# Optimization experiments

Hardware: AMD Instinct MI355X
Metric: run time of the kernel (lower is better)

Reference implementation:

```python
import jax, jax.numpy as jnp
import numpy as np

B, INDIM, ENC, BOT, DEC = 2048, 20000, 512, 128, 512
EPS = 1e-5


def _bn(x, g, b):
    # BatchNorm1d in training mode: biased batch stats
    m = jnp.mean(x, axis=0)
    v = jnp.mean(jnp.square(x - m), axis=0)
    return (x - m) * jax.lax.rsqrt(v + EPS) * g + b


def setup_inputs() -> dict:
    key = jax.random.key(0)
    ks = jax.random.split(key, 8)
    s = 0.02  # small init scale keeps exp() outputs finite
    return {
        "x": jax.random.uniform(ks[0], (B, INDIM), dtype=jnp.float32),
        "bn0_g": jnp.ones((INDIM,), jnp.float32),
        "bn0_b": jnp.zeros((INDIM,), jnp.float32),
        "enc_W": jax.random.normal(ks[1], (ENC, INDIM), jnp.float32) * s,
        "enc_b": jnp.zeros((ENC,), jnp.float32),
        "bn1_g": jnp.ones((ENC,), jnp.float32),
        "bn1_b": jnp.zeros((ENC,), jnp.float32),
        "bot_W": jax.random.normal(ks[2], (BOT, ENC), jnp.float32) * s,
        "bot_b": jnp.zeros((BOT,), jnp.float32),
        "bn2_g": jnp.ones((BOT,), jnp.float32),
        "bn2_b": jnp.zeros((BOT,), jnp.float32),
        "dec_W": jax.random.normal(ks[3], (DEC, BOT), jnp.float32) * s,
        "dec_b": jnp.zeros((DEC,), jnp.float32),
        "o1_W": jax.random.normal(ks[4], (INDIM, DEC), jnp.float32) * s,
        "o1_b": jnp.zeros((INDIM,), jnp.float32),
        "o2_W": jax.random.normal(ks[5], (INDIM, DEC), jnp.float32) * s,
        "o2_b": jnp.zeros((INDIM,), jnp.float32),
        "o3_W": jax.random.normal(ks[6], (INDIM, DEC), jnp.float32) * s,
        "o3_b": jnp.zeros((INDIM,), jnp.float32),
    }


def reference(x, bn0_g, bn0_b, enc_W, enc_b, bn1_g, bn1_b, bot_W, bot_b,
              bn2_g, bn2_b, dec_W, dec_b, o1_W, o1_b, o2_W, o2_b, o3_W, o3_b):
    # row-sum / median normalization; diag-inverse @ x == x / s[:, None]
    row_sum = jnp.sum(x, axis=1)                     # [B]
    s = row_sum / jnp.median(row_sum)                # [B]
    h = jnp.log1p(x / s[:, None])                    # log(inv(diag(s)) @ x + 1)
    h = _bn(h, bn0_g, bn0_b)
    h = jax.nn.relu(h @ enc_W.T + enc_b)
    h = _bn(h, bn1_g, bn1_b)
    h = jax.nn.relu(h @ bot_W.T + bot_b)
    h = _bn(h, bn2_g, bn2_b)
    h = jax.nn.relu(h @ dec_W.T + dec_b)
    M = jnp.exp(h @ o1_W.T + o1_b)
    M_loss = s[:, None] * M                          # diag(s) @ M
    pai = jax.nn.sigmoid(h @ o2_W.T + o2_b)
    theta = jnp.exp(h @ o3_W.T + o3_b)
    return pai, M, theta, M_loss
```

## Files before the change

kernel.cpp:

```cpp
#include <hip/hip_runtime.h>
#include <hip/hip_bf16.h>
#include <math.h>

#define B_    2048
#define IND   20000
#define ENCN  512
#define BOTN  128
#define DECN  512
#define KP1   20480
#define NP    20224
#define SPLITK 16
#define KSTEP1 20
#define BNEPS 1e-5f

typedef __hip_bfloat16 bf16;
typedef __bf16 bf16x8 __attribute__((ext_vector_type(8)));
typedef float f32x4 __attribute__((ext_vector_type(4)));
typedef unsigned short u16;

__device__ __forceinline__ u16 f2bfu(float f) {
  __hip_bfloat16 h = __float2bfloat16(f);
  return *reinterpret_cast<u16*>(&h);
}

__device__ __forceinline__ void gload_lds16(const bf16* g, bf16* l) {
  __builtin_amdgcn_global_load_lds(
      (const __attribute__((address_space(1))) void*)g,
      (__attribute__((address_space(3))) void*)l, 16, 0, 0);
}

__global__ void rowsum_k(const float* __restrict__ x, float* __restrict__ row_sum) {
  const int row = blockIdx.x;
  const f32x4* xr = (const f32x4*)(x + (size_t)row * IND);
  float s = 0.f;
  for (int i = threadIdx.x; i < IND / 4; i += 256) {
    f32x4 v = xr[i];
    s += (v[0] + v[1]) + (v[2] + v[3]);
  }
#pragma unroll
  for (int o = 32; o > 0; o >>= 1) s += __shfl_down(s, o, 64);
  __shared__ float ws4[4];
  if ((threadIdx.x & 63) == 0) ws4[threadIdx.x >> 6] = s;
  __syncthreads();
  if (threadIdx.x == 0) row_sum[row] = (ws4[0] + ws4[1]) + (ws4[2] + ws4[3]);
}

__global__ void median_scale_k(const float* __restrict__ row_sum,
                               float* __restrict__ sArr, float* __restrict__ invs) {
  __shared__ float v[B_];
  const int tid = threadIdx.x;
  v[tid] = row_sum[tid];
  v[tid + 1024] = row_sum[tid + 1024];
  __syncthreads();
  for (int k = 2; k <= B_; k <<= 1) {
    for (int j = k >> 1; j > 0; j >>= 1) {
      for (int i = tid; i < B_; i += 1024) {
        int ixj = i ^ j;
        if (ixj > i) {
          bool up = ((i & k) == 0);
          float a = v[i], b = v[ixj];
          if ((a > b) == up) { v[i] = b; v[ixj] = a; }
        }
      }
      __syncthreads();
    }
  }
  float med = 0.5f * (v[B_ / 2 - 1] + v[B_ / 2]);
  for (int i = tid; i < B_; i += 1024) {
    float rs = row_sum[i];
    sArr[i] = rs / med;
    invs[i] = med / rs;
  }
}

__global__ void pass2_k(const float* __restrict__ x, const float* __restrict__ invs,
                        bf16* __restrict__ L, float* __restrict__ part_s,
                        float* __restrict__ part_q) {
  const int c0 = (blockIdx.x * 256 + threadIdx.x) * 4;
  const int rblk = blockIdx.y;
  const int r0 = rblk * 32;
  const bool valid = (c0 < IND);
  f32x4 sum = {0.f, 0.f, 0.f, 0.f}, sq = {0.f, 0.f, 0.f, 0.f};
  for (int r = r0; r < r0 + 32; ++r) {
    f32x4 lv = {0.f, 0.f, 0.f, 0.f};
    if (valid) {
      f32x4 v = *(const f32x4*)(x + (size_t)r * IND + c0);
      float iv = invs[r];
      lv[0] = log1pf(v[0] * iv); lv[1] = log1pf(v[1] * iv);
      lv[2] = log1pf(v[2] * iv); lv[3] = log1pf(v[3] * iv);
      sum += lv; sq += lv * lv;
    }
    ushort4 o;
    o.x = f2bfu(lv[0]); o.y = f2bfu(lv[1]); o.z = f2bfu(lv[2]); o.w = f2bfu(lv[3]);
    *(ushort4*)((u16*)L + (size_t)r * KP1 + c0) = o;
  }
  if (valid) {
    *(f32x4*)(part_s + (size_t)rblk * KP1 + c0) = sum;
    *(f32x4*)(part_q + (size_t)rblk * KP1 + c0) = sq;
  }
}

__global__ void finalize_bn_k(const float* __restrict__ part_s, const float* __restrict__ part_q,
                              const float* __restrict__ g, const float* __restrict__ b,
                              float* __restrict__ scale, float* __restrict__ shift) {
  int c = blockIdx.x * 256 + threadIdx.x;
  if (c >= IND) return;
  float s = 0.f, q = 0.f;
  for (int z = 0; z < 64; ++z) {
    s += part_s[(size_t)z * KP1 + c];
    q += part_q[(size_t)z * KP1 + c];
  }
  const float invN = 1.f / (float)B_;
  float mean = s * invN;
  float var = q * invN - mean * mean;
  float sc = g[c] * rsqrtf(var + BNEPS);
  scale[c] = sc;
  shift[c] = b[c] - mean * sc;
}

__global__ void prepw_k(const float* __restrict__ encW, const float* __restrict__ enc_b,
                        const float* __restrict__ scale0, const float* __restrict__ shift0,
                        bf16* __restrict__ Wp, float* __restrict__ bias1) {
  const int e = blockIdx.x;
  float local = 0.f;
  for (int j0 = threadIdx.x * 4; j0 < KP1; j0 += 1024) {
    ushort4 o;
    if (j0 < IND) {
      f32x4 w = *(const f32x4*)(encW + (size_t)e * IND + j0);
      f32x4 sc = *(const f32x4*)(scale0 + j0);
      f32x4 sh = *(const f32x4*)(shift0 + j0);
      local += sh[0] * w[0] + sh[1] * w[1] + sh[2] * w[2] + sh[3] * w[3];
      o.x = f2bfu(w[0] * sc[0]); o.y = f2bfu(w[1] * sc[1]);
      o.z = f2bfu(w[2] * sc[2]); o.w = f2bfu(w[3] * sc[3]);
    } else {
      o.x = 0; o.y = 0; o.z = 0; o.w = 0;
    }
    *(ushort4*)((u16*)Wp + (size_t)e * KP1 + j0) = o;
  }
#pragma unroll
  for (int o = 32; o > 0; o >>= 1) local += __shfl_down(local, o, 64);
  __shared__ float red[4];
  if ((threadIdx.x & 63) == 0) red[threadIdx.x >> 6] = local;
  __syncthreads();
  if (threadIdx.x == 0) bias1[e] = enc_b[e] + ((red[0] + red[1]) + (red[2] + red[3]));
}

template <int MODE>
__global__ __launch_bounds__(512, 2)
void gemm256(const bf16* __restrict__ A, const bf16* __restrict__ Bm,
             int Kpad, int ksteps,
             float* __restrict__ out0, float* __restrict__ out1,
             const float* __restrict__ bias, const float* __restrict__ sArr,
             int ldo, int Nlimit) {
  extern __shared__ __align__(16) bf16 smem[];
  bf16* AsB = smem;
  bf16* BsB = smem + 32768;
  const int tid = threadIdx.x;
  const int lane = tid & 63;
  const int wave = tid >> 6;
  const int wr = wave >> 2;
  const int wc = wave & 3;

  const int nwg = gridDim.x;
  const int q8 = nwg >> 3;
  const int bid = blockIdx.x;
  const int swz = (bid & 7) * q8 + (bid >> 3);
  const int xm = swz & 7;
  const int rest = swz >> 3;
  int yn, z;
  if (MODE == 0) { yn = rest & 1; z = rest >> 1; } else { yn = rest; z = 0; }
  const int m0 = xm * 256;
  const int n0 = yn * 256;
  const int kbeg = z * ksteps * 64;

  const int srow = tid >> 3;
  const int schunk = (tid & 7) ^ (srow & 7);
  const bf16* gA = A + (size_t)(m0 + srow) * Kpad + kbeg + schunk * 8;
  const bf16* gB = Bm + (size_t)(n0 + srow) * Kpad + kbeg + schunk * 8;
  const int ldst = tid * 8;

  f32x4 acc[8][4] = {};
  const int lrow = lane & 15;
  const int kq = lane >> 4;

  auto STAGE = [&](int ks, int buf) {
    const bf16* ga = gA + (size_t)ks * 64;
    const bf16* gb = gB + (size_t)ks * 64;
    bf16* la = AsB + buf * 16384 + ldst;
    bf16* lb = BsB + buf * 16384 + ldst;
#pragma unroll
    for (int i = 0; i < 4; ++i) {
      gload_lds16(ga + (size_t)(i * 64) * Kpad, la + i * 4096);
      gload_lds16(gb + (size_t)(i * 64) * Kpad, lb + i * 4096);
    }
  };

  STAGE(0, 0);
  asm volatile("s_waitcnt vmcnt(0)" ::: "memory");
  __builtin_amdgcn_s_barrier();

  int cur = 0;
  for (int ks = 0; ks < ksteps; ++ks) {
    if (ks + 1 < ksteps) STAGE(ks + 1, cur ^ 1);
    const bf16* As = AsB + cur * 16384;
    const bf16* Bs = BsB + cur * 16384;
#pragma unroll
    for (int kk = 0; kk < 2; ++kk) {
      const int kc = kk * 4 + kq;
      bf16x8 af[8], bfv[4];
#pragma unroll
      for (int m = 0; m < 8; ++m) {
        const int row = wr * 128 + m * 16 + lrow;
        af[m] = *(const bf16x8*)(&As[row * 64 + ((kc ^ (row & 7)) << 3)]);
      }
#pragma unroll
      for (int n = 0; n < 4; ++n) {
        const int row = wc * 64 + n * 16 + lrow;
        bfv[n] = *(const bf16x8*)(&Bs[row * 64 + ((kc ^ (row & 7)) << 3)]);
      }
#pragma unroll
      for (int m = 0; m < 8; ++m)
#pragma unroll
        for (int n = 0; n < 4; ++n)
          acc[m][n] = __builtin_amdgcn_mfma_f32_16x16x32_bf16(bfv[n], af[m], acc[m][n], 0, 0, 0);
    }
    if (ks + 1 < ksteps) {
      asm volatile("s_waitcnt vmcnt(0)" ::: "memory");
      __builtin_amdgcn_s_barrier();
      cur ^= 1;
    }
  }

  float* o0 = out0;
  if (MODE == 0) o0 += (size_t)z * ((size_t)B_ * ldo);
  const int growb = m0 + wr * 128 + lrow;
  const int gcolb = n0 + wc * 64 + kq * 4;
#pragma unroll
  for (int m = 0; m < 8; ++m) {
    const int grow = growb + m * 16;
    float srow_s = 0.f;
    if (MODE == 2) srow_s = sArr[grow];
#pragma unroll
    for (int n = 0; n < 4; ++n) {
      const int gcol = gcolb + n * 16;
      f32x4 v = acc[m][n];
      if (MODE == 0) {
        *(f32x4*)(&o0[(size_t)grow * ldo + gcol]) = v;
      } else if (gcol < Nlimit) {
        f32x4 bb = *(const f32x4*)(&bias[gcol]);
        f32x4 t = v + bb;
        f32x4 r;
        if (MODE == 1) {
#pragma unroll
          for (int j = 0; j < 4; ++j) r[j] = 1.f / (1.f + __expf(-t[j]));
          *(f32x4*)(&o0[(size_t)grow * ldo + gcol]) = r;
        } else if (MODE == 2) {
#pragma unroll
          for (int j = 0; j < 4; ++j) r[j] = __expf(t[j]);
          *(f32x4*)(&o0[(size_t)grow * ldo + gcol]) = r;
          f32x4 rl;
#pragma unroll
          for (int j = 0; j < 4; ++j) rl[j] = srow_s * r[j];
          *(f32x4*)(&out1[(size_t)grow * ldo + gcol]) = rl;
        } else {
#pragma unroll
          for (int j = 0; j < 4; ++j) r[j] = __expf(t[j]);
          *(f32x4*)(&o0[(size_t)grow * ldo + gcol]) = r;
        }
      }
    }
  }
}

template <int MODE>
__global__ __launch_bounds__(256, 2)
void gemm128(const bf16* __restrict__ A, const bf16* __restrict__ Bm,
             int Kpad, int ksteps,
             float* __restrict__ outF, bf16* __restrict__ outB,
             const float* __restrict__ bias, int ldo) {
  __shared__ __align__(16) bf16 As[2][128 * 64];
  __shared__ __align__(16) bf16 Bs[2][128 * 64];
  const int tid = threadIdx.x;
  const int wave = tid >> 6;
  const int lane = tid & 63;
  const int wr = wave >> 1, wc = wave & 1;
  const int m0 = blockIdx.x * 128;
  const int n0 = blockIdx.y * 128;

  const int srow = wave * 32 + (lane >> 3);
  const int scol = ((lane & 7) ^ (lane >> 3)) * 8;
  const bf16* gA = A + (size_t)(m0 + srow) * Kpad + scol;
  const bf16* gB = Bm + (size_t)(n0 + srow) * Kpad + scol;
  const int lbase = wave * 2048;

  f32x4 acc[4][4] = {};
  const int lrow = lane & 15;
  const int swz = lrow & 7;
  const int kq = lane >> 4;

  auto STAGE = [&](int ks, int buf) {
    const bf16* ga = gA + (size_t)ks * 64;
    const bf16* gb = gB + (size_t)ks * 64;
#pragma unroll
    for (int i = 0; i < 4; ++i) {
      gload_lds16(ga + (size_t)(i * 8) * Kpad, &As[buf][lbase + i * 512]);
      gload_lds16(gb + (size_t)(i * 8) * Kpad, &Bs[buf][lbase + i * 512]);
    }
  };

  STAGE(0, 0);
  asm volatile("s_waitcnt vmcnt(0)" ::: "memory");
  __builtin_amdgcn_s_barrier();

  int cur = 0;
  for (int ks = 0; ks < ksteps; ++ks) {
    if (ks + 1 < ksteps) STAGE(ks + 1, cur ^ 1);
#pragma unroll
    for (int kk = 0; kk < 2; ++kk) {
      const int kc = kk * 4 + kq;
      bf16x8 af[4], bfv[4];
#pragma unroll
      for (int m = 0; m < 4; ++m) {
        const int row = wr * 64 + m * 16 + lrow;
        af[m] = *(const bf16x8*)(&As[cur][row * 64 + (((kc ^ swz) & 7) << 3)]);
      }
#pragma unroll
      for (int n = 0; n < 4; ++n) {
        const int row = wc * 64 + n * 16 + lrow;
        bfv[n] = *(const bf16x8*)(&Bs[cur][row * 64 + (((kc ^ swz) & 7) << 3)]);
      }
#pragma unroll
      for (int m = 0; m < 4; ++m)
#pragma unroll
        for (int n = 0; n < 4; ++n)
          acc[m][n] = __builtin_amdgcn_mfma_f32_16x16x32_bf16(bfv[n], af[m], acc[m][n], 0, 0, 0);
    }
    if (ks + 1 < ksteps) {
      asm volatile("s_waitcnt vmcnt(0)" ::: "memory");
      __builtin_amdgcn_s_barrier();
      cur ^= 1;
    }
  }

  const int growb = m0 + wr * 64 + lrow;
  const int gcolb = n0 + wc * 64 + kq * 4;
#pragma unroll
  for (int m = 0; m < 4; ++m) {
    const int grow = growb + m * 16;
#pragma unroll
    for (int n = 0; n < 4; ++n) {
      const int gcol = gcolb + n * 16;
      f32x4 bb = *(const f32x4*)(&bias[gcol]);
      f32x4 t = acc[m][n] + bb;
      if (MODE == 4) {
        f32x4 r;
#pragma unroll
        for (int j = 0; j < 4; ++j) r[j] = fmaxf(t[j], 0.f);
        *(f32x4*)(&outF[(size_t)grow * ldo + gcol]) = r;
      } else {
        ushort4 o;
        o.x = f2bfu(fmaxf(t[0], 0.f)); o.y = f2bfu(fmaxf(t[1], 0.f));
        o.z = f2bfu(fmaxf(t[2], 0.f)); o.w = f2bfu(fmaxf(t[3], 0.f));
        *(ushort4*)((u16*)outB + (size_t)grow * ldo + gcol) = o;
      }
    }
  }
}

__global__ void reduce1_k(const float* __restrict__ Cp, const float* __restrict__ bias1,
                          float* __restrict__ C1) {
  const size_t i4 = ((size_t)blockIdx.x * 256 + threadIdx.x) * 4;
  f32x4 t = {0.f, 0.f, 0.f, 0.f};
#pragma unroll
  for (int z = 0; z < SPLITK; ++z) t += *(const f32x4*)(Cp + (size_t)z * (B_ * ENCN) + i4);
  f32x4 bb = *(const f32x4*)(bias1 + (i4 & (ENCN - 1)));
  t += bb;
  f32x4 r;
#pragma unroll
  for (int j = 0; j < 4; ++j) r[j] = fmaxf(t[j], 0.f);
  *(f32x4*)(C1 + i4) = r;
}

__global__ void colpart_k(const float* __restrict__ X, int C,
                          float* __restrict__ ps, float* __restrict__ pq) {
  const int cl = threadIdx.x & 63;
  const int rg = threadIdx.x >> 6;
  const int c = blockIdx.x * 64 + cl;
  const int r0 = blockIdx.y * 64 + rg * 16;
  float sum = 0.f, sq = 0.f;
  for (int rr = 0; rr < 16; ++rr) {
    float v = X[(size_t)(r0 + rr) * C + c];
    sum += v; sq += v * v;
  }
  __shared__ float ls[4][64], lq[4][64];
  ls[rg][cl] = sum; lq[rg][cl] = sq;
  __syncthreads();
  if (rg == 0) {
    sum = (ls[0][cl] + ls[1][cl]) + (ls[2][cl] + ls[3][cl]);
    sq = (lq[0][cl] + lq[1][cl]) + (lq[2][cl] + lq[3][cl]);
    ps[(size_t)blockIdx.y * C + c] = sum;
    pq[(size_t)blockIdx.y * C + c] = sq;
  }
}

__global__ void colfin_k(const float* __restrict__ ps, const float* __restrict__ pq,
                         const float* __restrict__ g, const float* __restrict__ b,
                         float* __restrict__ scale, float* __restrict__ shift, int C) {
  int c = blockIdx.x * 256 + threadIdx.x;
  if (c >= C) return;
  float sum = 0.f, sq = 0.f;
  for (int z = 0; z < 32; ++z) {
    sum += ps[(size_t)z * C + c];
    sq += pq[(size_t)z * C + c];
  }
  const float invN = 1.f / (float)B_;
  float mean = sum * invN;
  float var = sq * invN - mean * mean;
  float sc = g[c] * rsqrtf(var + BNEPS);
  scale[c] = sc;
  shift[c] = b[c] - mean * sc;
}

__global__ void affine_k(const float* __restrict__ X, const float* __restrict__ sc,
                         const float* __restrict__ sh, bf16* __restrict__ out, int Cm1) {
  const size_t i4 = ((size_t)blockIdx.x * 256 + threadIdx.x) * 4;
  const int c0 = (int)(i4 & (size_t)Cm1);
  f32x4 v = *(const f32x4*)(X + i4);
  f32x4 s = *(const f32x4*)(sc + c0);
  f32x4 h = *(const f32x4*)(sh + c0);
  f32x4 t = v * s + h;
  ushort4 o;
  o.x = f2bfu(t[0]); o.y = f2bfu(t[1]); o.z = f2bfu(t[2]); o.w = f2bfu(t[3]);
  *(ushort4*)((u16*)out + i4) = o;
}

__global__ void cvtw_k(const float* __restrict__ src, bf16* __restrict__ dst) {
  const size_t i4 = ((size_t)blockIdx.x * 256 + threadIdx.x) * 4;
  f32x4 v = *(const f32x4*)(src + i4);
  ushort4 o;
  o.x = f2bfu(v[0]); o.y = f2bfu(v[1]); o.z = f2bfu(v[2]); o.w = f2bfu(v[3]);
  *(ushort4*)((u16*)dst + i4) = o;
}

__global__ void cvt_o_k(const float* __restrict__ Wsrc, bf16* __restrict__ Wb) {
  const size_t idx = ((size_t)blockIdx.x * 256 + threadIdx.x) * 4;
  const int e = (int)(idx >> 9);
  ushort4 o;
  if (e < IND) {
    f32x4 v = *(const f32x4*)(Wsrc + idx);
    o.x = f2bfu(v[0]); o.y = f2bfu(v[1]); o.z = f2bfu(v[2]); o.w = f2bfu(v[3]);
  } else {
    o.x = 0; o.y = 0; o.z = 0; o.w = 0;
  }
  *(ushort4*)((u16*)Wb + idx) = o;
}

extern "C" void kernel_launch(void* const* d_in, const int* in_sizes, int n_in,
                              void* d_out, int out_size, void* d_ws, size_t ws_size,
                              hipStream_t stream) {
  const float* x     = (const float*)d_in[0];
  const float* bn0_g = (const float*)d_in[1];
  const float* bn0_b = (const float*)d_in[2];
  const float* enc_W = (const float*)d_in[3];
  const float* enc_b = (const float*)d_in[4];
  const float* bn1_g = (const float*)d_in[5];
  const float* bn1_b = (const float*)d_in[6];
  const float* bot_W = (const float*)d_in[7];
  const float* bot_b = (const float*)d_in[8];
  const float* bn2_g = (const float*)d_in[9];
  const float* bn2_b = (const float*)d_in[10];
  const float* dec_W = (const float*)d_in[11];
  const float* dec_b = (const float*)d_in[12];
  const float* o1_W  = (const float*)d_in[13];
  const float* o1_b  = (const float*)d_in[14];
  const float* o2_W  = (const float*)d_in[15];
  const float* o2_b  = (const float*)d_in[16];
  const float* o3_W  = (const float*)d_in[17];
  const float* o3_b  = (const float*)d_in[18];

  char* wsb = (char*)d_ws;
  size_t off = 0;
  auto alloc = [&](size_t bytes) -> void* {
    void* p = wsb + off;
    off = (off + bytes + 255) & ~(size_t)255;
    return p;
  };
  float* row_sum = (float*)alloc(B_ * 4);
  float* sArr    = (float*)alloc(B_ * 4);
  float* invs    = (float*)alloc(B_ * 4);
  float* scale0  = (float*)alloc(IND * 4);
  float* shift0  = (float*)alloc(IND * 4);
  float* bias1   = (float*)alloc(ENCN * 4);
  float* scale1  = (float*)alloc(ENCN * 4);
  float* shift1  = (float*)alloc(ENCN * 4);
  float* scale2  = (float*)alloc(BOTN * 4);
  float* shift2  = (float*)alloc(BOTN * 4);
  float* ps1     = (float*)alloc(32 * ENCN * 4);
  float* pq1     = (float*)alloc(32 * ENCN * 4);
  float* ps2     = (float*)alloc(32 * BOTN * 4);
  float* pq2     = (float*)alloc(32 * BOTN * 4);
  float* C1      = (float*)alloc((size_t)B_ * ENCN * 4);
  float* C2f     = (float*)alloc((size_t)B_ * BOTN * 4);
  float* Cp      = (float*)alloc((size_t)SPLITK * B_ * ENCN * 4);
  bf16*  L       = (bf16*)alloc((size_t)B_ * KP1 * 2);
  bf16*  Wp      = (bf16*)alloc((size_t)ENCN * KP1 * 2);
  bf16*  A1b     = (bf16*)alloc((size_t)B_ * ENCN * 2);
  bf16*  A2b     = (bf16*)alloc((size_t)B_ * BOTN * 2);
  bf16*  botWb   = (bf16*)alloc((size_t)BOTN * ENCN * 2);
  bf16*  decWb   = (bf16*)alloc((size_t)DECN * BOTN * 2);
  bf16*  h3      = (bf16*)alloc((size_t)B_ * DECN * 2);
  bf16*  wbf0    = (bf16*)alloc((size_t)NP * 512 * 2);
  bf16*  wbf1    = (bf16*)alloc((size_t)NP * 512 * 2);
  bf16*  wbf2    = (bf16*)alloc((size_t)NP * 512 * 2);
  float* part_s  = Cp;
  float* part_q  = Cp + (size_t)64 * KP1;

  hipFuncSetAttribute(reinterpret_cast<const void*>(gemm256<0>),
                      hipFuncAttributeMaxDynamicSharedMemorySize, 131072);
  hipFuncSetAttribute(reinterpret_cast<const void*>(gemm256<1>),
                      hipFuncAttributeMaxDynamicSharedMemorySize, 131072);
  hipFuncSetAttribute(reinterpret_cast<const void*>(gemm256<2>),
                      hipFuncAttributeMaxDynamicSharedMemorySize, 131072);
  hipFuncSetAttribute(reinterpret_cast<const void*>(gemm256<3>),
                      hipFuncAttributeMaxDynamicSharedMemorySize, 131072);

  rowsum_k<<<B_, 256, 0, stream>>>(x, row_sum);
  median_scale_k<<<1, 1024, 0, stream>>>(row_sum, sArr, invs);

  pass2_k<<<dim3(KP1 / 1024, 64), 256, 0, stream>>>(x, invs, L, part_s, part_q);
  finalize_bn_k<<<(IND + 255) / 256, 256, 0, stream>>>(part_s, part_q, bn0_g, bn0_b,
                                                       scale0, shift0);

  prepw_k<<<ENCN, 256, 0, stream>>>(enc_W, enc_b, scale0, shift0, Wp, bias1);

  gemm256<0><<<8 * 2 * SPLITK, 512, 131072, stream>>>(
      L, Wp, KP1, KSTEP1, Cp, nullptr, nullptr, nullptr, ENCN, ENCN);
  reduce1_k<<<(B_ * ENCN) / 1024, 256, 0, stream>>>(Cp, bias1, C1);

  colpart_k<<<dim3(ENCN / 64, 32), 256, 0, stream>>>(C1, ENCN, ps1, pq1);
  colfin_k<<<2, 256, 0, stream>>>(ps1, pq1, bn1_g, bn1_b, scale1, shift1, ENCN);
  affine_k<<<(B_ * ENCN) / 1024, 256, 0, stream>>>(C1, scale1, shift1, A1b, ENCN - 1);
  cvtw_k<<<(BOTN * ENCN) / 1024, 256, 0, stream>>>(bot_W, botWb);
  gemm128<4><<<dim3(16, 1), 256, 0, stream>>>(A1b, botWb, ENCN, ENCN / 64,
                                              C2f, nullptr, bot_b, BOTN);
  colpart_k<<<dim3(BOTN / 64, 32), 256, 0, stream>>>(C2f, BOTN, ps2, pq2);
  colfin_k<<<1, 256, 0, stream>>>(ps2, pq2, bn2_g, bn2_b, scale2, shift2, BOTN);
  affine_k<<<(B_ * BOTN) / 1024, 256, 0, stream>>>(C2f, scale2, shift2, A2b, BOTN - 1);
  cvtw_k<<<(DECN * BOTN) / 1024, 256, 0, stream>>>(dec_W, decWb);
  gemm128<5><<<dim3(16, 4), 256, 0, stream>>>(A2b, decWb, BOTN, BOTN / 64,
                                              nullptr, h3, dec_b, DECN);

  const int cvtg = (NP * 512) / 1024;
  cvt_o_k<<<cvtg, 256, 0, stream>>>(o1_W, wbf0);
  cvt_o_k<<<cvtg, 256, 0, stream>>>(o2_W, wbf1);
  cvt_o_k<<<cvtg, 256, 0, stream>>>(o3_W, wbf2);

  float* out = (float*)d_out;
  const size_t OFF = (size_t)B_ * IND;
  const int onwg = 8 * (NP / 256);
  gemm256<1><<<onwg, 512, 131072, stream>>>(
      h3, wbf1, 512, 8, out, nullptr, o2_b, nullptr, IND, IND);
  gemm256<2><<<onwg, 512, 131072, stream>>>(
      h3, wbf0, 512, 8, out + OFF, out + 3 * OFF, o1_b, sArr, IND, IND);
  gemm256<3><<<onwg, 512, 131072, stream>>>(
      h3, wbf2, 512, 8, out + 2 * OFF, nullptr, o3_b, nullptr, IND, IND);
}
```

Measured before the change: 677.1 us.

## Fuse weight conversion into GEMMs, merge output GEMMs, fuse BN stats into reductions

The three output GEMMs become one launch of 1896 workgroups. That launch reads the fp32 weights directly and converts them to bf16 while staging them in LDS, so the separate conversion passes and their bf16 weight buffers are gone. The mid-layer GEMMs also read fp32 activations and weights, applying the batch-norm affine and the bf16 conversion in the staging step, and the bottleneck GEMM gains a split-K of 4. The split-K reductions now compute the column sum and sum-of-squares directly, which replaces colpart and affine and removes many small launches. In exchange, B staging goes through registers instead of direct global-to-LDS loads, and each fp32 weight tile is converted again by every workgroup that reads it.

```diff
diff --git a/kernel.cpp b/kernel.cpp
--- a/kernel.cpp
+++ b/kernel.cpp
@@ -11,6 +11,7 @@
 #define NP    20224
 #define SPLITK 16
 #define KSTEP1 20
+#define SPLITK2 4
 #define BNEPS 1e-5f
 
 typedef __hip_bfloat16 bf16;
@@ -21,6 +22,13 @@
 __device__ __forceinline__ u16 f2bfu(float f) {
   __hip_bfloat16 h = __float2bfloat16(f);
   return *reinterpret_cast<u16*>(&h);
+}
+
+__device__ __forceinline__ void st_b64_bf16(void* p, f32x4 v) {
+  union { u16 u[4]; uint2 d; } o;
+  o.u[0] = f2bfu(v[0]); o.u[1] = f2bfu(v[1]);
+  o.u[2] = f2bfu(v[2]); o.u[3] = f2bfu(v[3]);
+  *(uint2*)p = o.d;
 }
 
 __device__ __forceinline__ void gload_lds16(const bf16* g, bf16* l) {
@@ -145,13 +153,9 @@
   if (threadIdx.x == 0) bias1[e] = enc_b[e] + ((red[0] + red[1]) + (red[2] + red[3]));
 }
 
-template <int MODE>
 __global__ __launch_bounds__(512, 2)
-void gemm256(const bf16* __restrict__ A, const bf16* __restrict__ Bm,
-             int Kpad, int ksteps,
-             float* __restrict__ out0, float* __restrict__ out1,
-             const float* __restrict__ bias, const float* __restrict__ sArr,
-             int ldo, int Nlimit) {
+void gemm1_k(const bf16* __restrict__ A, const bf16* __restrict__ Bm,
+             float* __restrict__ Cp) {
   extern __shared__ __align__(16) bf16 smem[];
   bf16* AsB = smem;
   bf16* BsB = smem + 32768;
@@ -161,22 +165,20 @@
   const int wr = wave >> 2;
   const int wc = wave & 3;
 
-  const int nwg = gridDim.x;
-  const int q8 = nwg >> 3;
   const int bid = blockIdx.x;
-  const int swz = (bid & 7) * q8 + (bid >> 3);
+  const int swz = (bid & 7) * 32 + (bid >> 3);
   const int xm = swz & 7;
   const int rest = swz >> 3;
-  int yn, z;
-  if (MODE == 0) { yn = rest & 1; z = rest >> 1; } else { yn = rest; z = 0; }
+  const int yn = rest & 1;
+  const int z = rest >> 1;
   const int m0 = xm * 256;
   const int n0 = yn * 256;
-  const int kbeg = z * ksteps * 64;
+  const int kbeg = z * KSTEP1 * 64;
 
   const int srow = tid >> 3;
   const int schunk = (tid & 7) ^ (srow & 7);
-  const bf16* gA = A + (size_t)(m0 + srow) * Kpad + kbeg + schunk * 8;
-  const bf16* gB = Bm + (size_t)(n0 + srow) * Kpad + kbeg + schunk * 8;
+  const bf16* gA = A + (size_t)(m0 + srow) * KP1 + kbeg + schunk * 8;
+  const bf16* gB = Bm + (size_t)(n0 + srow) * KP1 + kbeg + schunk * 8;
   const int ldst = tid * 8;
 
   f32x4 acc[8][4] = {};
@@ -190,8 +192,8 @@
     bf16* lb = BsB + buf * 16384 + ldst;
 #pragma unroll
     for (int i = 0; i < 4; ++i) {
-      gload_lds16(ga + (size_t)(i * 64) * Kpad, la + i * 4096);
-      gload_lds16(gb + (size_t)(i * 64) * Kpad, lb + i * 4096);
+      gload_lds16(ga + (size_t)(i * 64) * KP1, la + i * 4096);
+      gload_lds16(gb + (size_t)(i * 64) * KP1, lb + i * 4096);
     }
   };
 
@@ -200,8 +202,8 @@
   __builtin_amdgcn_s_barrier();
 
   int cur = 0;
-  for (int ks = 0; ks < ksteps; ++ks) {
-    if (ks + 1 < ksteps) STAGE(ks + 1, cur ^ 1);
+  for (int ks = 0; ks < KSTEP1; ++ks) {
+    if (ks + 1 < KSTEP1) STAGE(ks + 1, cur ^ 1);
     const bf16* As = AsB + cur * 16384;
     const bf16* Bs = BsB + cur * 16384;
 #pragma unroll
@@ -224,97 +226,203 @@
         for (int n = 0; n < 4; ++n)
           acc[m][n] = __builtin_amdgcn_mfma_f32_16x16x32_bf16(bfv[n], af[m], acc[m][n], 0, 0, 0);
     }
-    if (ks + 1 < ksteps) {
+    if (ks + 1 < KSTEP1) {
       asm volatile("s_waitcnt vmcnt(0)" ::: "memory");
       __builtin_amdgcn_s_barrier();
       cur ^= 1;
     }
   }
 
-  float* o0 = out0;
-  if (MODE == 0) o0 += (size_t)z * ((size_t)B_ * ldo);
+  float* o0 = Cp + (size_t)z * ((size_t)B_ * ENCN);
   const int growb = m0 + wr * 128 + lrow;
   const int gcolb = n0 + wc * 64 + kq * 4;
 #pragma unroll
   for (int m = 0; m < 8; ++m) {
     const int grow = growb + m * 16;
-    float srow_s = 0.f;
-    if (MODE == 2) srow_s = sArr[grow];
 #pragma unroll
     for (int n = 0; n < 4; ++n) {
       const int gcol = gcolb + n * 16;
-      f32x4 v = acc[m][n];
-      if (MODE == 0) {
-        *(f32x4*)(&o0[(size_t)grow * ldo + gcol]) = v;
-      } else if (gcol < Nlimit) {
-        f32x4 bb = *(const f32x4*)(&bias[gcol]);
-        f32x4 t = v + bb;
+      *(f32x4*)(&o0[(size_t)grow * ENCN + gcol]) = acc[m][n];
+    }
+  }
+}
+
+__global__ __launch_bounds__(512, 2)
+void gemm_out_k(const bf16* __restrict__ h3,
+                const float* __restrict__ W0, const float* __restrict__ W1,
+                const float* __restrict__ W2,
+                const float* __restrict__ b0, const float* __restrict__ b1,
+                const float* __restrict__ b2,
+                const float* __restrict__ sArr, float* __restrict__ out) {
+  extern __shared__ __align__(16) bf16 smem[];
+  bf16* AsB = smem;
+  bf16* BsB = smem + 32768;
+  const int tid = threadIdx.x;
+  const int lane = tid & 63;
+  const int wave = tid >> 6;
+  const int wr = wave >> 2;
+  const int wc = wave & 3;
+
+  const int bid = blockIdx.x;
+  const int swz = (bid & 7) * 237 + (bid >> 3);
+  const int g = swz / 632;
+  const int r2 = swz - g * 632;
+  const int xm = r2 & 7;
+  const int yn = r2 >> 3;
+  const int m0 = xm * 256;
+  const int n0 = yn * 256;
+
+  const float* Wg = (g == 0) ? W0 : (g == 1) ? W1 : W2;
+  const float* bg = (g == 0) ? b0 : (g == 1) ? b1 : b2;
+  const size_t OFF = (size_t)B_ * IND;
+  float* o0 = out + (size_t)g * OFF;
+  float* o1 = out + 3 * OFF;
+
+  const int srow = tid >> 3;
+  const int schunk = (tid & 7) ^ (srow & 7);
+  const bf16* gA = h3 + (size_t)(m0 + srow) * ENCN + schunk * 8;
+  const int ldstA = tid * 8;
+
+  const int lrow = lane & 15;
+  const int kq = lane >> 4;
+  const int bcol = lrow * 4;
+  const int brow0 = wave * 32 + kq;
+
+  f32x4 acc[8][4] = {};
+  f32x4 bv[8];
+
+  auto LOADA = [&](int ks, int buf) {
+    const bf16* ga = gA + ks * 64;
+    bf16* la = AsB + buf * 16384 + ldstA;
+#pragma unroll
+    for (int i = 0; i < 4; ++i)
+      gload_lds16(ga + (size_t)(i * 64) * ENCN, la + i * 4096);
+  };
+  auto LOADB = [&](int ks) {
+#pragma unroll
+    for (int i = 0; i < 8; ++i) {
+      const int gr = n0 + brow0 + i * 4;
+      if (gr < IND) bv[i] = *(const f32x4*)(Wg + (size_t)gr * ENCN + ks * 64 + bcol);
+      else bv[i] = f32x4{0.f, 0.f, 0.f, 0.f};
+    }
+  };
+  auto WRITEB = [&](int buf) {
+    char* lb = (char*)(BsB + buf * 16384);
+#pragma unroll
+    for (int i = 0; i < 8; ++i) {
+      const int r = brow0 + i * 4;
+      const int byte = r * 128 + (((lrow >> 1) ^ (r & 7)) << 4) + ((lrow & 1) << 3);
+      st_b64_bf16(lb + byte, bv[i]);
+    }
+  };
+
+  LOADB(0);
+  LOADA(0, 0);
+  WRITEB(0);
+  __syncthreads();
+
+  int cur = 0;
+  for (int ks = 0; ks < 8; ++ks) {
+    if (ks < 7) { LOADA(ks + 1, cur ^ 1); LOADB(ks + 1); }
+    const bf16* As = AsB + cur * 16384;
+    const bf16* Bs = BsB + cur * 16384;
+#pragma unroll
+    for (int kk = 0; kk < 2; ++kk) {
+      const int kc = kk * 4 + kq;
+      bf16x8 af[8], bfv[4];
+#pragma unroll
+      for (int m = 0; m < 8; ++m) {
+        const int row = wr * 128 + m * 16 + lrow;
+        af[m] = *(const bf16x8*)(&As[row * 64 + ((kc ^ (row & 7)) << 3)]);
+      }
+#pragma unroll
+      for (int n = 0; n < 4; ++n) {
+        const int row = wc * 64 + n * 16 + lrow;
+        bfv[n] = *(const bf16x8*)(&Bs[row * 64 + ((kc ^ (row & 7)) << 3)]);
+      }
+#pragma unroll
+      for (int m = 0; m < 8; ++m)
+#pragma unroll
+        for (int n = 0; n < 4; ++n)
+          acc[m][n] = __builtin_amdgcn_mfma_f32_16x16x32_bf16(bfv[n], af[m], acc[m][n], 0, 0, 0);
+    }
+    if (ks < 7) {
+      WRITEB(cur ^ 1);
+      __syncthreads();
+      cur ^= 1;
+    }
+  }
+
+  const int growb = m0 + wr * 128 + lrow;
+  const int gcolb = n0 + wc * 64 + kq * 4;
+#pragma unroll
+  for (int m = 0; m < 8; ++m) {
+    const int grow = growb + m * 16;
+    float ss = (g == 1) ? sArr[grow] : 0.f;
+#pragma unroll
+    for (int n = 0; n < 4; ++n) {
+      const int gcol = gcolb + n * 16;
+      if (gcol < IND) {
+        f32x4 t = acc[m][n] + *(const f32x4*)(&bg[gcol]);
         f32x4 r;
-        if (MODE == 1) {
+        if (g == 0) {
 #pragma unroll
           for (int j = 0; j < 4; ++j) r[j] = 1.f / (1.f + __expf(-t[j]));
-          *(f32x4*)(&o0[(size_t)grow * ldo + gcol]) = r;
-        } else if (MODE == 2) {
+          *(f32x4*)(&o0[(size_t)grow * IND + gcol]) = r;
+        } else {
 #pragma unroll
           for (int j = 0; j < 4; ++j) r[j] = __expf(t[j]);
-          *(f32x4*)(&o0[(size_t)grow * ldo + gcol]) = r;
-          f32x4 rl;
-#pragma unroll
-          for (int j = 0; j < 4; ++j) rl[j] = srow_s * r[j];
-          *(f32x4*)(&out1[(size_t)grow * ldo + gcol]) = rl;
-        } else {
-#pragma unroll
-          for (int j = 0; j < 4; ++j) r[j] = __expf(t[j]);
-          *(f32x4*)(&o0[(size_t)grow * ldo + gcol]) = r;
+          *(f32x4*)(&o0[(size_t)grow * IND + gcol]) = r;
+          if (g == 1) {
+            f32x4 rl;
+#pragma unroll
+            for (int j = 0; j < 4; ++j) rl[j] = ss * r[j];
+            *(f32x4*)(&o1[(size_t)grow * IND + gcol]) = rl;
+          }
         }
       }
     }
   }
 }
 
-template <int MODE>
+template <int EPI>
 __global__ __launch_bounds__(256, 2)
-void gemm128(const bf16* __restrict__ A, const bf16* __restrict__ Bm,
-             int Kpad, int ksteps,
-             float* __restrict__ outF, bf16* __restrict__ outB,
-             const float* __restrict__ bias, int ldo) {
-  __shared__ __align__(16) bf16 As[2][128 * 64];
-  __shared__ __align__(16) bf16 Bs[2][128 * 64];
+void gemm_mid_k(const float* __restrict__ A, int lda,
+                const float* __restrict__ scl, const float* __restrict__ sft,
+                const float* __restrict__ W, int ldb,
+                const float* __restrict__ bias,
+                float* __restrict__ outP, bf16* __restrict__ outB, int ldo) {
+  __shared__ __align__(16) bf16 As[128 * 64];
+  __shared__ __align__(16) bf16 Bs[128 * 64];
   const int tid = threadIdx.x;
+  const int lane = tid & 63;
   const int wave = tid >> 6;
-  const int lane = tid & 63;
   const int wr = wave >> 1, wc = wave & 1;
   const int m0 = blockIdx.x * 128;
   const int n0 = blockIdx.y * 128;
-
-  const int srow = wave * 32 + (lane >> 3);
-  const int scol = ((lane & 7) ^ (lane >> 3)) * 8;
-  const bf16* gA = A + (size_t)(m0 + srow) * Kpad + scol;
-  const bf16* gB = Bm + (size_t)(n0 + srow) * Kpad + scol;
-  const int lbase = wave * 2048;
+  const int z = blockIdx.z;
+  const int kbeg = z * 128;
+  const int lrow = lane & 15;
+  const int kq = lane >> 4;
+  const int scol = lrow * 4;
+  const int srow0 = wave * 32 + kq;
 
   f32x4 acc[4][4] = {};
-  const int lrow = lane & 15;
-  const int swz = lrow & 7;
-  const int kq = lane >> 4;
-
-  auto STAGE = [&](int ks, int buf) {
-    const bf16* ga = gA + (size_t)ks * 64;
-    const bf16* gb = gB + (size_t)ks * 64;
-#pragma unroll
-    for (int i = 0; i < 4; ++i) {
-      gload_lds16(ga + (size_t)(i * 8) * Kpad, &As[buf][lbase + i * 512]);
-      gload_lds16(gb + (size_t)(i * 8) * Kpad, &Bs[buf][lbase + i * 512]);
-    }
-  };
-
-  STAGE(0, 0);
-  asm volatile("s_waitcnt vmcnt(0)" ::: "memory");
-  __builtin_amdgcn_s_barrier();
-
-  int cur = 0;
-  for (int ks = 0; ks < ksteps; ++ks) {
-    if (ks + 1 < ksteps) STAGE(ks + 1, cur ^ 1);
+  for (int ks = 0; ks < 2; ++ks) {
+    const int kb = kbeg + ks * 64;
+    f32x4 sc4 = *(const f32x4*)(scl + kb + scol);
+    f32x4 sf4 = *(const f32x4*)(sft + kb + scol);
+#pragma unroll
+    for (int i = 0; i < 8; ++i) {
+      const int r = srow0 + i * 4;
+      const int byte = r * 128 + (((lrow >> 1) ^ (r & 7)) << 4) + ((lrow & 1) << 3);
+      f32x4 a = *(const f32x4*)(A + (size_t)(m0 + r) * lda + kb + scol);
+      a = a * sc4 + sf4;
+      st_b64_bf16((char*)As + byte, a);
+      f32x4 b = *(const f32x4*)(W + (size_t)(n0 + r) * ldb + kb + scol);
+      st_b64_bf16((char*)Bs + byte, b);
+    }
+    __syncthreads();
 #pragma unroll
     for (int kk = 0; kk < 2; ++kk) {
       const int kc = kk * 4 + kq;
@@ -322,12 +430,12 @@
 #pragma unroll
       for (int m = 0; m < 4; ++m) {
         const int row = wr * 64 + m * 16 + lrow;
-        af[m] = *(const bf16x8*)(&As[cur][row * 64 + (((kc ^ swz) & 7) << 3)]);
+        af[m] = *(const bf16x8*)(&As[row * 64 + ((kc ^ (row & 7)) << 3)]);
       }
 #pragma unroll
       for (int n = 0; n < 4; ++n) {
         const int row = wc * 64 + n * 16 + lrow;
-        bfv[n] = *(const bf16x8*)(&Bs[cur][row * 64 + (((kc ^ swz) & 7) << 3)]);
+        bfv[n] = *(const bf16x8*)(&Bs[row * 64 + ((kc ^ (row & 7)) << 3)]);
       }
 #pragma unroll
       for (int m = 0; m < 4; ++m)
@@ -335,11 +443,7 @@
         for (int n = 0; n < 4; ++n)
           acc[m][n] = __builtin_amdgcn_mfma_f32_16x16x32_bf16(bfv[n], af[m], acc[m][n], 0, 0, 0);
     }
-    if (ks + 1 < ksteps) {
-      asm volatile("s_waitcnt vmcnt(0)" ::: "memory");
-      __builtin_amdgcn_s_barrier();
-      cur ^= 1;
-    }
+    __syncthreads();
   }
 
   const int growb = m0 + wr * 64 + lrow;
@@ -350,109 +454,114 @@
 #pragma unroll
     for (int n = 0; n < 4; ++n) {
       const int gcol = gcolb + n * 16;
-      f32x4 bb = *(const f32x4*)(&bias[gcol]);
-      f32x4 t = acc[m][n] + bb;
-      if (MODE == 4) {
+      if (EPI == 0) {
+        float* op = outP + (size_t)z * ((size_t)B_ * ldo);
+        *(f32x4*)(&op[(size_t)grow * ldo + gcol]) = acc[m][n];
+      } else {
+        f32x4 t = acc[m][n] + *(const f32x4*)(&bias[gcol]);
         f32x4 r;
 #pragma unroll
         for (int j = 0; j < 4; ++j) r[j] = fmaxf(t[j], 0.f);
-        *(f32x4*)(&outF[(size_t)grow * ldo + gcol]) = r;
-      } else {
-        ushort4 o;
-        o.x = f2bfu(fmaxf(t[0], 0.f)); o.y = f2bfu(fmaxf(t[1], 0.f));
-        o.z = f2bfu(fmaxf(t[2], 0.f)); o.w = f2bfu(fmaxf(t[3], 0.f));
-        *(ushort4*)((u16*)outB + (size_t)grow * ldo + gcol) = o;
-      }
-    }
-  }
-}
-
-__global__ void reduce1_k(const float* __restrict__ Cp, const float* __restrict__ bias1,
-                          float* __restrict__ C1) {
-  const size_t i4 = ((size_t)blockIdx.x * 256 + threadIdx.x) * 4;
-  f32x4 t = {0.f, 0.f, 0.f, 0.f};
-#pragma unroll
-  for (int z = 0; z < SPLITK; ++z) t += *(const f32x4*)(Cp + (size_t)z * (B_ * ENCN) + i4);
-  f32x4 bb = *(const f32x4*)(bias1 + (i4 & (ENCN - 1)));
-  t += bb;
-  f32x4 r;
-#pragma unroll
-  for (int j = 0; j < 4; ++j) r[j] = fmaxf(t[j], 0.f);
-  *(f32x4*)(C1 + i4) = r;
-}
-
-__global__ void colpart_k(const float* __restrict__ X, int C,
-                          float* __restrict__ ps, float* __restrict__ pq) {
-  const int cl = threadIdx.x & 63;
-  const int rg = threadIdx.x >> 6;
-  const int c = blockIdx.x * 64 + cl;
-  const int r0 = blockIdx.y * 64 + rg * 16;
-  float sum = 0.f, sq = 0.f;
-  for (int rr = 0; rr < 16; ++rr) {
-    float v = X[(size_t)(r0 + rr) * C + c];
-    sum += v; sq += v * v;
-  }
-  __shared__ float ls[4][64], lq[4][64];
-  ls[rg][cl] = sum; lq[rg][cl] = sq;
+        st_b64_bf16((u16*)outB + (size_t)grow * ldo + gcol, r);
+      }
+    }
+  }
+}
+
+__global__ void reduce1c_k(const float* __restrict__ Cp, const float* __restrict__ bias1,
+                           float* __restrict__ C1, float* __restrict__ ps,
+                           float* __restrict__ pq) {
+  const int b = blockIdx.x;
+  const int t = threadIdx.x;
+  const int c4 = (t & 127) * 4;
+  const int rs = t >> 7;
+  f32x4 bb = *(const f32x4*)(bias1 + c4);
+  f32x4 sum = {0.f, 0.f, 0.f, 0.f}, sq = {0.f, 0.f, 0.f, 0.f};
+#pragma unroll
+  for (int rr = 0; rr < 4; ++rr) {
+    const int row = b * 8 + rs + rr * 2;
+    f32x4 v = {0.f, 0.f, 0.f, 0.f};
+#pragma unroll
+    for (int z = 0; z < SPLITK; ++z)
+      v += *(const f32x4*)(Cp + (size_t)z * (B_ * ENCN) + (size_t)row * ENCN + c4);
+    v += bb;
+    f32x4 r;
+#pragma unroll
+    for (int j = 0; j < 4; ++j) r[j] = fmaxf(v[j], 0.f);
+    *(f32x4*)(C1 + (size_t)row * ENCN + c4) = r;
+    sum += r; sq += r * r;
+  }
+  __shared__ f32x4 ls[2][128], lq[2][128];
+  ls[rs][t & 127] = sum; lq[rs][t & 127] = sq;
   __syncthreads();
-  if (rg == 0) {
-    sum = (ls[0][cl] + ls[1][cl]) + (ls[2][cl] + ls[3][cl]);
-    sq = (lq[0][cl] + lq[1][cl]) + (lq[2][cl] + lq[3][cl]);
-    ps[(size_t)blockIdx.y * C + c] = sum;
-    pq[(size_t)blockIdx.y * C + c] = sq;
+  if (t < 128) {
+    f32x4 s = ls[0][t] + ls[1][t];
+    f32x4 q = lq[0][t] + lq[1][t];
+    *(f32x4*)(ps + (size_t)b * ENCN + t * 4) = s;
+    *(f32x4*)(pq + (size_t)b * ENCN + t * 4) = q;
+  }
+}
+
+__global__ void reduce2c_k(const float* __restrict__ Cp2, const float* __restrict__ bias,
+                           float* __restrict__ C2, float* __restrict__ ps,
+                           float* __restrict__ pq) {
+  const int b = blockIdx.x;
+  const int t = threadIdx.x;
+  const int c4 = (t & 31) * 4;
+  const int rs = t >> 5;
+  f32x4 bb = *(const f32x4*)(bias + c4);
+  f32x4 sum = {0.f, 0.f, 0.f, 0.f}, sq = {0.f, 0.f, 0.f, 0.f};
+#pragma unroll
+  for (int rr = 0; rr < 2; ++rr) {
+    const int row = b * 16 + rs + rr * 8;
+    f32x4 v = {0.f, 0.f, 0.f, 0.f};
+#pragma unroll
+    for (int z = 0; z < SPLITK2; ++z)
+      v += *(const f32x4*)(Cp2 + (size_t)z * (B_ * BOTN) + (size_t)row * BOTN + c4);
+    v += bb;
+    f32x4 r;
+#pragma unroll
+    for (int j = 0; j < 4; ++j) r[j] = fmaxf(v[j], 0.f);
+    *(f32x4*)(C2 + (size_t)row * BOTN + c4) = r;
+    sum += r; sq += r * r;
+  }
+  __shared__ f32x4 ls[8][32], lq[8][32];
+  ls[rs][t & 31] = sum; lq[rs][t & 31] = sq;
+  __syncthreads();
+  if (t < 32) {
+    f32x4 s = {0.f, 0.f, 0.f, 0.f}, q = {0.f, 0.f, 0.f, 0.f};
+#pragma unroll
+    for (int k = 0; k < 8; ++k) { s += ls[k][t]; q += lq[k][t]; }
+    *(f32x4*)(ps + (size_t)b * BOTN + t * 4) = s;
+    *(f32x4*)(pq + (size_t)b * BOTN + t * 4) = q;
   }
 }
 
 __global__ void colfin_k(const float* __restrict__ ps, const float* __restrict__ pq,
                          const float* __restrict__ g, const float* __restrict__ b,
-                         float* __restrict__ scale, float* __restrict__ shift, int C) {
-  int c = blockIdx.x * 256 + threadIdx.x;
-  if (c >= C) return;
-  float sum = 0.f, sq = 0.f;
-  for (int z = 0; z < 32; ++z) {
-    sum += ps[(size_t)z * C + c];
-    sq += pq[(size_t)z * C + c];
-  }
-  const float invN = 1.f / (float)B_;
-  float mean = sum * invN;
-  float var = sq * invN - mean * mean;
-  float sc = g[c] * rsqrtf(var + BNEPS);
-  scale[c] = sc;
-  shift[c] = b[c] - mean * sc;
-}
-
-__global__ void affine_k(const float* __restrict__ X, const float* __restrict__ sc,
-                         const float* __restrict__ sh, bf16* __restrict__ out, int Cm1) {
-  const size_t i4 = ((size_t)blockIdx.x * 256 + threadIdx.x) * 4;
-  const int c0 = (int)(i4 & (size_t)Cm1);
-  f32x4 v = *(const f32x4*)(X + i4);
-  f32x4 s = *(const f32x4*)(sc + c0);
-  f32x4 h = *(const f32x4*)(sh + c0);
-  f32x4 t = v * s + h;
-  ushort4 o;
-  o.x = f2bfu(t[0]); o.y = f2bfu(t[1]); o.z = f2bfu(t[2]); o.w = f2bfu(t[3]);
-  *(ushort4*)((u16*)out + i4) = o;
-}
-
-__global__ void cvtw_k(const float* __restrict__ src, bf16* __restrict__ dst) {
-  const size_t i4 = ((size_t)blockIdx.x * 256 + threadIdx.x) * 4;
-  f32x4 v = *(const f32x4*)(src + i4);
-  ushort4 o;
-  o.x = f2bfu(v[0]); o.y = f2bfu(v[1]); o.z = f2bfu(v[2]); o.w = f2bfu(v[3]);
-  *(ushort4*)((u16*)dst + i4) = o;
-}
-
-__global__ void cvt_o_k(const float* __restrict__ Wsrc, bf16* __restrict__ Wb) {
-  const size_t idx = ((size_t)blockIdx.x * 256 + threadIdx.x) * 4;
-  const int e = (int)(idx >> 9);
-  ushort4 o;
-  if (e < IND) {
-    f32x4 v = *(const f32x4*)(Wsrc + idx);
-    o.x = f2bfu(v[0]); o.y = f2bfu(v[1]); o.z = f2bfu(v[2]); o.w = f2bfu(v[3]);
-  } else {
-    o.x = 0; o.y = 0; o.z = 0; o.w = 0;
-  }
-  *(ushort4*)((u16*)Wb + idx) = o;
+                         float* __restrict__ scale, float* __restrict__ shift,
+                         int C, int nPart) {
+  const int cl = threadIdx.x & 63;
+  const int pg = threadIdx.x >> 6;
+  const int c = blockIdx.x * 64 + cl;
+  float s = 0.f, q = 0.f;
+  for (int p = pg; p < nPart; p += 4) {
+    s += ps[(size_t)p * C + c];
+    q += pq[(size_t)p * C + c];
+  }
+  __shared__ float ls[4][64], lq[4][64];
+  ls[pg][cl] = s; lq[pg][cl] = q;
+  __syncthreads();
+  if (pg == 0) {
+    s = (ls[0][cl] + ls[1][cl]) + (ls[2][cl] + ls[3][cl]);
+    q = (lq[0][cl] + lq[1][cl]) + (lq[2][cl] + lq[3][cl]);
+    const float invN = 1.f / (float)B_;
+    float mean = s * invN;
+    float var = q * invN - mean * mean;
+    float sc = g[c] * rsqrtf(var + BNEPS);
+    scale[c] = sc;
+    shift[c] = b[c] - mean * sc;
+  }
 }
 
 extern "C" void kernel_launch(void* const* d_in, const int* in_sizes, int n_in,
@@ -495,33 +604,23 @@
   float* shift1  = (float*)alloc(ENCN * 4);
   float* scale2  = (float*)alloc(BOTN * 4);
   float* shift2  = (float*)alloc(BOTN * 4);
-  float* ps1     = (float*)alloc(32 * ENCN * 4);
-  float* pq1     = (float*)alloc(32 * ENCN * 4);
-  float* ps2     = (float*)alloc(32 * BOTN * 4);
-  float* pq2     = (float*)alloc(32 * BOTN * 4);
+  float* ps1     = (float*)alloc(256 * ENCN * 4);
+  float* pq1     = (float*)alloc(256 * ENCN * 4);
+  float* ps2     = (float*)alloc(128 * BOTN * 4);
+  float* pq2     = (float*)alloc(128 * BOTN * 4);
   float* C1      = (float*)alloc((size_t)B_ * ENCN * 4);
   float* C2f     = (float*)alloc((size_t)B_ * BOTN * 4);
+  float* Cp2     = (float*)alloc((size_t)SPLITK2 * B_ * BOTN * 4);
   float* Cp      = (float*)alloc((size_t)SPLITK * B_ * ENCN * 4);
   bf16*  L       = (bf16*)alloc((size_t)B_ * KP1 * 2);
   bf16*  Wp      = (bf16*)alloc((size_t)ENCN * KP1 * 2);
-  bf16*  A1b     = (bf16*)alloc((size_t)B_ * ENCN * 2);
-  bf16*  A2b     = (bf16*)alloc((size_t)B_ * BOTN * 2);
-  bf16*  botWb   = (bf16*)alloc((size_t)BOTN * ENCN * 2);
-  bf16*  decWb   = (bf16*)alloc((size_t)DECN * BOTN * 2);
   bf16*  h3      = (bf16*)alloc((size_t)B_ * DECN * 2);
-  bf16*  wbf0    = (bf16*)alloc((size_t)NP * 512 * 2);
-  bf16*  wbf1    = (bf16*)alloc((size_t)NP * 512 * 2);
-  bf16*  wbf2    = (bf16*)alloc((size_t)NP * 512 * 2);
   float* part_s  = Cp;
   float* part_q  = Cp + (size_t)64 * KP1;
 
-  hipFuncSetAttribute(reinterpret_cast<const void*>(gemm256<0>),
+  hipFuncSetAttribute(reinterpret_cast<const void*>(gemm1_k),
                       hipFuncAttributeMaxDynamicSharedMemorySize, 131072);
-  hipFuncSetAttribute(reinterpret_cast<const void*>(gemm256<1>),
-                      hipFuncAttributeMaxDynamicSharedMemorySize, 131072);
-  hipFuncSetAttribute(reinterpret_cast<const void*>(gemm256<2>),
-                      hipFuncAttributeMaxDynamicSharedMemorySize, 131072);
-  hipFuncSetAttribute(reinterpret_cast<const void*>(gemm256<3>),
+  hipFuncSetAttribute(reinterpret_cast<const void*>(gemm_out_k),
                       hipFuncAttributeMaxDynamicSharedMemorySize, 131072);
 
   rowsum_k<<<B_, 256, 0, stream>>>(x, row_sum);
@@ -533,35 +632,20 @@
 
   prepw_k<<<ENCN, 256, 0, stream>>>(enc_W, enc_b, scale0, shift0, Wp, bias1);
 
-  gemm256<0><<<8 * 2 * SPLITK, 512, 131072, stream>>>(
-      L, Wp, KP1, KSTEP1, Cp, nullptr, nullptr, nullptr, ENCN, ENCN);
-  reduce1_k<<<(B_ * ENCN) / 1024, 256, 0, stream>>>(Cp, bias1, C1);
-
-  colpart_k<<<dim3(ENCN / 64, 32), 256, 0, stream>>>(C1, ENCN, ps1, pq1);
-  colfin_k<<<2, 256, 0, stream>>>(ps1, pq1, bn1_g, bn1_b, scale1, shift1, ENCN);
-  affine_k<<<(B_ * ENCN) / 1024, 256, 0, stream>>>(C1, scale1, shift1, A1b, ENCN - 1);
-  cvtw_k<<<(BOTN * ENCN) / 1024, 256, 0, stream>>>(bot_W, botWb);
-  gemm128<4><<<dim3(16, 1), 256, 0, stream>>>(A1b, botWb, ENCN, ENCN / 64,
-                                              C2f, nullptr, bot_b, BOTN);
-  colpart_k<<<dim3(BOTN / 64, 32), 256, 0, stream>>>(C2f, BOTN, ps2, pq2);
-  colfin_k<<<1, 256, 0, stream>>>(ps2, pq2, bn2_g, bn2_b, scale2, shift2, BOTN);
-  affine_k<<<(B_ * BOTN) / 1024, 256, 0, stream>>>(C2f, scale2, shift2, A2b, BOTN - 1);
-  cvtw_k<<<(DECN * BOTN) / 1024, 256, 0, stream>>>(dec_W, decWb);
-  gemm128<5><<<dim3(16, 4), 256, 0, stream>>>(A2b, decWb, BOTN, BOTN / 64,
-                                              nullptr, h3, dec_b, DECN);
-
-  const int cvtg = (NP * 512) / 1024;
-  cvt_o_k<<<cvtg, 256, 0, stream>>>(o1_W, wbf0);
-  cvt_o_k<<<cvtg, 256, 0, stream>>>(o2_W, wbf1);
-  cvt_o_k<<<cvtg, 256, 0, stream>>>(o3_W, wbf2);
+  gemm1_k<<<256, 512, 131072, stream>>>(L, Wp, Cp);
+  reduce1c_k<<<256, 256, 0, stream>>>(Cp, bias1, C1, ps1, pq1);
+  colfin_k<<<ENCN / 64, 256, 0, stream>>>(ps1, pq1, bn1_g, bn1_b, scale1, shift1,
+                                          ENCN, 256);
+
+  gemm_mid_k<0><<<dim3(16, 1, SPLITK2), 256, 0, stream>>>(
+      C1, ENCN, scale1, shift1, bot_W, ENCN, nullptr, Cp2, nullptr, BOTN);
+  reduce2c_k<<<128, 256, 0, stream>>>(Cp2, bot_b, C2f, ps2, pq2);
+  colfin_k<<<BOTN / 64, 256, 0, stream>>>(ps2, pq2, bn2_g, bn2_b, scale2, shift2,
+                                          BOTN, 128);
+  gemm_mid_k<1><<<dim3(16, 4, 1), 256, 0, stream>>>(
+      C2f, BOTN, scale2, shift2, dec_W, BOTN, dec_b, nullptr, h3, DECN);
 
   float* out = (float*)d_out;
-  const size_t OFF = (size_t)B_ * IND;
-  const int onwg = 8 * (NP / 256);
-  gemm256<1><<<onwg, 512, 131072, stream>>>(
-      h3, wbf1, 512, 8, out, nullptr, o2_b, nullptr, IND, IND);
-  gemm256<2><<<onwg, 512, 131072, stream>>>(
-      h3, wbf0, 512, 8, out + OFF, out + 3 * OFF, o1_b, sArr, IND, IND);
-  gemm256<3><<<onwg, 512, 131072, stream>>>(
-      h3, wbf2, 512, 8, out + 2 * OFF, nullptr, o3_b, nullptr, IND, IND);
-}
+  gemm_out_k<<<1896, 512, 131072, stream>>>(h3, o2_W, o1_W, o3_W,
+                                            o2_b, o1_b, o3_b, sArr, out);
+}
```

Result: slower. 728.3 us (+7.6%).
